# Performance work log

Measured on AMD Instinct MI355X. Metric: run time of the kernel, lower is better.

## Reference

```python
import jax, jax.numpy as jnp
import numpy as np

DIM = 1024
N = 65536

def _l2norm(x):
    # F.normalize: x / max(||x||_2, eps) along last dim, eps=1e-12
    n = jnp.linalg.norm(x, axis=-1, keepdims=True)
    return x / jnp.maximum(n, 1e-12)

def setup_inputs() -> dict:
    key = jax.random.key(0)
    ks = jax.random.split(key, 10)
    s = 0.02
    return {
        "q_init": jax.random.normal(ks[0], (1, DIM), jnp.float32),
        "k_init": jax.random.normal(ks[1], (N, DIM), jnp.float32),
        "Wq": jax.random.normal(ks[2], (DIM, DIM // 2), jnp.float32) * s,
        "bq": jnp.zeros((DIM // 2,), jnp.float32),
        "Wk": jax.random.normal(ks[3], (DIM, DIM // 2), jnp.float32) * s,
        "bk": jnp.zeros((DIM // 2,), jnp.float32),
        "Wv": jax.random.normal(ks[4], (DIM, DIM), jnp.float32) * s,
        "bv": jnp.zeros((DIM,), jnp.float32),
        "Wm": jax.random.normal(ks[5], (DIM, DIM), jnp.float32) * s,
        "bm": jnp.zeros((DIM,), jnp.float32),
        "gamma": jnp.ones((1,), jnp.float32),
    }

def reference(q_init, k_init, Wq, bq, Wk, bk, Wv, bv, Wm, bm, gamma):
    q = _l2norm(q_init) @ Wq + bq              # [1, dim/2]
    kn = _l2norm(k_init)                        # [N, dim]
    k = kn @ Wk + bk                            # [N, dim/2]
    v = kn @ Wv + bv                            # [N, dim]
    scores = q @ k.T                            # [1, N]
    # global mean/std rescale (torch.std is unbiased, ddof=1)
    scores = (scores - scores.mean()) / (jnp.std(scores, ddof=1) + 1e-8)
    attn = jax.nn.softmax(jnp.clip(scores, -10.0, 10.0), axis=-1)
    # dropout is identity in eval mode
    out = (attn @ v) @ Wm + bm                  # [1, dim]
    g = jax.nn.sigmoid(gamma)                   # [1]
    return g * q_init + (1.0 - g) * out
```

## Files before the change

kernel.cpp:

```cpp
#include <hip/hip_runtime.h>
#include <math.h>

#define DIM   1024
#define HALF  512
#define NROWS 65536
#define SBLK  4096
#define WBLK  2048
#define WF1   64

#define OFF_SCAL   0
#define OFF_QACC   (OFF_SCAL + 8)
#define OFF_PVEC   (OFF_QACC + HALF)
#define OFF_PSTAT  (OFF_PVEC + DIM)
#define OFF_S      (OFF_PSTAT + 2*SBLK)
#define OFF_INVN   (OFF_S + NROWS)
#define OFF_PESUM  (OFF_INVN + NROWS)
#define OFF_PW     (OFF_PESUM + WBLK)
#define OFF_P2     (OFF_PW + WBLK*DIM)
#define OFF_WACC   (OFF_P2 + WF1*DIM)
#define OFF_OVACC  (OFF_WACC + DIM)
#define OFF_END    (OFF_OVACC + DIM)

__global__ void k_prep(const float* __restrict__ q_init,
                       const float* __restrict__ Wq,
                       float* __restrict__ qacc) {
    __shared__ float qs[DIM];
    __shared__ float4 red4[256];
    __shared__ float red[256];
    int t = threadIdx.x, c4 = blockIdx.x;
    float sq = 0.f;
    #pragma unroll
    for (int i = 0; i < 4; ++i) {
        float v = q_init[t + i * 256];
        qs[t + i * 256] = v;
        sq += v * v;
    }
    red[t] = sq;
    __syncthreads();
    for (int s = 128; s > 0; s >>= 1) {
        if (t < s) red[t] += red[t + s];
        __syncthreads();
    }
    float inv = 1.0f / fmaxf(sqrtf(red[0]), 1e-12f);
    const float4* W4 = (const float4*)Wq;
    float4 acc = make_float4(0.f, 0.f, 0.f, 0.f);
    for (int r = t; r < DIM; r += 256) {
        float c = qs[r] * inv;
        float4 m = W4[(size_t)r * (HALF / 4) + c4];
        acc.x += c * m.x; acc.y += c * m.y; acc.z += c * m.z; acc.w += c * m.w;
    }
    red4[t] = acc;
    __syncthreads();
    for (int s = 128; s > 0; s >>= 1) {
        if (t < s) {
            red4[t].x += red4[t + s].x; red4[t].y += red4[t + s].y;
            red4[t].z += red4[t + s].z; red4[t].w += red4[t + s].w;
        }
        __syncthreads();
    }
    if (t == 0) ((float4*)qacc)[c4] = red4[0];
}

__global__ void k_pvec(const float* __restrict__ Wk,
                       const float* __restrict__ qacc,
                       const float* __restrict__ bq,
                       float* __restrict__ pvec) {
    __shared__ float q[HALF];
    int t = threadIdx.x;
    for (int j = t; j < HALF; j += 256) q[j] = qacc[j] + bq[j];
    __syncthreads();
    int wave = t >> 6, lane = t & 63;
    int d = blockIdx.x * 4 + wave;
    const float* row = Wk + (size_t)d * HALF;
    float acc = 0.f;
    #pragma unroll
    for (int j0 = 0; j0 < HALF; j0 += 64) acc += row[j0 + lane] * q[j0 + lane];
    #pragma unroll
    for (int o = 32; o > 0; o >>= 1) acc += __shfl_down(acc, o);
    if (lane == 0) pvec[d] = acc;
}

__global__ void k_scores(const float* __restrict__ K,
                         const float* __restrict__ pvec,
                         float* __restrict__ svals,
                         float* __restrict__ invn,
                         float2* __restrict__ pstat) {
    __shared__ float4 p4s[256];
    __shared__ float wsum[4], wssq[4];
    int t = threadIdx.x;
    p4s[t] = ((const float4*)pvec)[t];
    __syncthreads();
    int wave = t >> 6, lane = t & 63;
    int row0 = blockIdx.x * 16 + wave * 4;
    const float4* k4 = (const float4*)K + (size_t)row0 * 256 + lane;
    float4 v[16];
    #pragma unroll
    for (int r = 0; r < 4; ++r)
        #pragma unroll
        for (int i = 0; i < 4; ++i)
            v[r * 4 + i] = k4[r * 256 + i * 64];
    float d[4] = {0, 0, 0, 0}, q[4] = {0, 0, 0, 0};
    #pragma unroll
    for (int r = 0; r < 4; ++r) {
        #pragma unroll
        for (int i = 0; i < 4; ++i) {
            float4 a = v[r * 4 + i];
            float4 p = p4s[lane + i * 64];
            d[r] += a.x * p.x + a.y * p.y + a.z * p.z + a.w * p.w;
            q[r] += a.x * a.x + a.y * a.y + a.z * a.z + a.w * a.w;
        }
    }
    #pragma unroll
    for (int o = 32; o > 0; o >>= 1) {
        #pragma unroll
        for (int r = 0; r < 4; ++r) {
            d[r] += __shfl_down(d[r], o);
            q[r] += __shfl_down(q[r], o);
        }
    }
    if (lane == 0) {
        float i0 = 1.0f / fmaxf(sqrtf(q[0]), 1e-12f);
        float i1 = 1.0f / fmaxf(sqrtf(q[1]), 1e-12f);
        float i2 = 1.0f / fmaxf(sqrtf(q[2]), 1e-12f);
        float i3 = 1.0f / fmaxf(sqrtf(q[3]), 1e-12f);
        float s0 = d[0] * i0, s1 = d[1] * i1, s2 = d[2] * i2, s3 = d[3] * i3;
        *(float4*)(svals + row0) = make_float4(s0, s1, s2, s3);
        *(float4*)(invn + row0) = make_float4(i0, i1, i2, i3);
        wsum[wave] = s0 + s1 + s2 + s3;
        wssq[wave] = s0 * s0 + s1 * s1 + s2 * s2 + s3 * s3;
    }
    __syncthreads();
    if (t == 0)
        pstat[blockIdx.x] = make_float2(wsum[0] + wsum[1] + wsum[2] + wsum[3],
                                        wssq[0] + wssq[1] + wssq[2] + wssq[3]);
}

__global__ void k_redstats(const float2* __restrict__ pstat, float* __restrict__ scal) {
    __shared__ float rs[1024], rq[1024];
    int t = threadIdx.x;
    float s = 0.f, q = 0.f;
    for (int i = t; i < SBLK; i += 1024) {
        float2 p = pstat[i];
        s += p.x; q += p.y;
    }
    rs[t] = s; rq[t] = q;
    __syncthreads();
    for (int k = 512; k > 0; k >>= 1) {
        if (t < k) { rs[t] += rs[t + k]; rq[t] += rq[t + k]; }
        __syncthreads();
    }
    if (t == 0) {
        float mean = rs[0] / (float)NROWS;
        float var  = (rq[0] - (float)NROWS * mean * mean) / (float)(NROWS - 1);
        scal[0] = mean;
        scal[1] = 1.0f / (sqrtf(fmaxf(var, 0.0f)) + 1e-8f);
    }
}

__global__ void k_wsum(const float* __restrict__ K,
                       const float* __restrict__ svals,
                       const float* __restrict__ invn,
                       const float* __restrict__ scal,
                       float* __restrict__ pw,
                       float* __restrict__ pesum) {
    int t = threadIdx.x;
    int b = (int)gridDim.x - 1 - (int)blockIdx.x;
    int r0 = b * 32;
    float mean = scal[0], rstd = scal[1];
    const float4* M4 = (const float4*)K + (size_t)r0 * 256 + t;
    float4 acc = make_float4(0.f, 0.f, 0.f, 0.f);
    float esum = 0.f;
    #pragma unroll
    for (int rb = 0; rb < 32; rb += 8) {
        float4 m[8];
        #pragma unroll
        for (int r = 0; r < 8; ++r) m[r] = M4[(size_t)(rb + r) * 256];
        #pragma unroll
        for (int r = 0; r < 8; ++r) {
            int ri = r0 + rb + r;
            float z = (svals[ri] - mean) * rstd;
            z = fminf(fmaxf(z, -10.0f), 10.0f);
            float e = expf(z);
            esum += e;
            float c = e * invn[ri];
            acc.x += c * m[r].x; acc.y += c * m[r].y;
            acc.z += c * m[r].z; acc.w += c * m[r].w;
        }
    }
    ((float4*)pw)[(size_t)b * 256 + t] = acc;
    if (t == 0) pesum[b] = esum;
}

__global__ void k_wfold(const float* __restrict__ pw, float* __restrict__ p2) {
    int t = threadIdx.x, b = blockIdx.x;
    const float4* pw4 = (const float4*)pw;
    float4 acc = make_float4(0.f, 0.f, 0.f, 0.f);
    #pragma unroll
    for (int p = 0; p < WBLK / WF1; ++p) {
        float4 m = pw4[(size_t)(b * (WBLK / WF1) + p) * 256 + t];
        acc.x += m.x; acc.y += m.y; acc.z += m.z; acc.w += m.w;
    }
    ((float4*)p2)[b * 256 + t] = acc;
}

__global__ void k_wreduce(const float* __restrict__ p2,
                          const float* __restrict__ pesum,
                          float* __restrict__ wacc) {
    __shared__ float red[1024];
    int t = threadIdx.x;
    float es = 0.f;
    for (int i = t; i < WBLK; i += 1024) es += pesum[i];
    red[t] = es;
    __syncthreads();
    for (int s = 512; s > 0; s >>= 1) {
        if (t < s) red[t] += red[t + s];
        __syncthreads();
    }
    float inv = 1.0f / red[0];
    float acc = 0.f;
    #pragma unroll
    for (int b = 0; b < WF1; ++b) acc += p2[b * DIM + t];
    wacc[t] = acc * inv;
}

__global__ void k_mv(const float* __restrict__ M,
                     const float* __restrict__ coeff,
                     const float* __restrict__ cbias,
                     float* __restrict__ out) {
    __shared__ float4 red[256];
    int t = threadIdx.x, c4 = blockIdx.x;
    const float4* M4 = (const float4*)M;
    float4 acc = make_float4(0.f, 0.f, 0.f, 0.f);
    for (int r = t; r < DIM; r += 256) {
        float c = coeff[r];
        if (cbias) c += cbias[r];
        float4 m = M4[(size_t)r * (DIM / 4) + c4];
        acc.x += c * m.x; acc.y += c * m.y; acc.z += c * m.z; acc.w += c * m.w;
    }
    red[t] = acc;
    __syncthreads();
    for (int s = 128; s > 0; s >>= 1) {
        if (t < s) {
            red[t].x += red[t + s].x; red[t].y += red[t + s].y;
            red[t].z += red[t + s].z; red[t].w += red[t + s].w;
        }
        __syncthreads();
    }
    if (t == 0) ((float4*)out)[c4] = red[0];
}

__global__ void k_mv_final(const float* __restrict__ M,
                           const float* __restrict__ coeff,
                           const float* __restrict__ cbias,
                           const float* __restrict__ q_init,
                           const float* __restrict__ bm,
                           const float* __restrict__ gamma,
                           float* __restrict__ out) {
    __shared__ float4 red[256];
    int t = threadIdx.x, c4 = blockIdx.x;
    const float4* M4 = (const float4*)M;
    float4 acc = make_float4(0.f, 0.f, 0.f, 0.f);
    for (int r = t; r < DIM; r += 256) {
        float c = coeff[r] + cbias[r];
        float4 m = M4[(size_t)r * (DIM / 4) + c4];
        acc.x += c * m.x; acc.y += c * m.y; acc.z += c * m.z; acc.w += c * m.w;
    }
    red[t] = acc;
    __syncthreads();
    for (int s = 128; s > 0; s >>= 1) {
        if (t < s) {
            red[t].x += red[t + s].x; red[t].y += red[t + s].y;
            red[t].z += red[t + s].z; red[t].w += red[t + s].w;
        }
        __syncthreads();
    }
    if (t == 0) {
        float g = 1.0f / (1.0f + expf(-gamma[0]));
        float4 qv = ((const float4*)q_init)[c4];
        float4 bmv = ((const float4*)bm)[c4];
        float4 o;
        o.x = g * qv.x + (1.0f - g) * (red[0].x + bmv.x);
        o.y = g * qv.y + (1.0f - g) * (red[0].y + bmv.y);
        o.z = g * qv.z + (1.0f - g) * (red[0].z + bmv.z);
        o.w = g * qv.w + (1.0f - g) * (red[0].w + bmv.w);
        ((float4*)out)[c4] = o;
    }
}

extern "C" void kernel_launch(void* const* d_in, const int* in_sizes, int n_in,
                              void* d_out, int out_size, void* d_ws, size_t ws_size,
                              hipStream_t stream) {
    const float* q_init = (const float*)d_in[0];
    const float* k_init = (const float*)d_in[1];
    const float* Wq     = (const float*)d_in[2];
    const float* bq     = (const float*)d_in[3];
    const float* Wk     = (const float*)d_in[4];
    const float* Wv     = (const float*)d_in[6];
    const float* bv     = (const float*)d_in[7];
    const float* Wm     = (const float*)d_in[8];
    const float* bm     = (const float*)d_in[9];
    const float* gamma  = (const float*)d_in[10];
    float* out = (float*)d_out;
    float* ws  = (float*)d_ws;

    float*  scal   = ws + OFF_SCAL;
    float*  qacc   = ws + OFF_QACC;
    float*  pvec   = ws + OFF_PVEC;
    float2* pstat  = (float2*)(ws + OFF_PSTAT);
    float*  svals  = ws + OFF_S;
    float*  invn   = ws + OFF_INVN;
    float*  pesum  = ws + OFF_PESUM;
    float*  pw     = ws + OFF_PW;
    float*  p2     = ws + OFF_P2;
    float*  wacc   = ws + OFF_WACC;
    float*  ovacc  = ws + OFF_OVACC;

    k_prep<<<HALF / 4, 256, 0, stream>>>(q_init, Wq, qacc);
    k_pvec<<<DIM / 4, 256, 0, stream>>>(Wk, qacc, bq, pvec);
    k_scores<<<SBLK, 256, 0, stream>>>(k_init, pvec, svals, invn, pstat);
    k_redstats<<<1, 1024, 0, stream>>>(pstat, scal);
    k_wsum<<<WBLK, 256, 0, stream>>>(k_init, svals, invn, scal, pw, pesum);
    k_wfold<<<WF1, 256, 0, stream>>>(pw, p2);
    k_wreduce<<<1, 1024, 0, stream>>>(p2, pesum, wacc);
    k_mv<<<DIM / 4, 256, 0, stream>>>(Wv, wacc, nullptr, ovacc);
    k_mv_final<<<DIM / 4, 256, 0, stream>>>(Wm, ovacc, bv, q_init, bm, gamma, out);
}
```

Measured before the change: 472.5 us.

## Fuse all stages into one cooperative persistent kernel with grid syncs

Replaces the nine-kernel pipeline with a single cooperative kernel of 512 blocks that separates the stages with grid.sync(). The scores and weighted-sum stages each process 128 rows per block, and the multi-level partial-sum folds collapse into one cross-block reduction. The aim is to remove launch overhead and intermediate round trips, and to keep the 256MB K matrix partly resident in cache between the two passes because each block rereads its own rows. In exchange it adds six grid-wide barriers and leaves fewer blocks in flight for hiding memory latency during the streaming passes.

```diff
diff --git a/kernel.cpp b/kernel.cpp
--- a/kernel.cpp
+++ b/kernel.cpp
@@ -1,289 +1,279 @@
 #include <hip/hip_runtime.h>
+#include <hip/hip_cooperative_groups.h>
 #include <math.h>
+
+namespace cg = cooperative_groups;
 
 #define DIM   1024
 #define HALF  512
 #define NROWS 65536
-#define SBLK  4096
-#define WBLK  2048
-#define WF1   64
-
-#define OFF_SCAL   0
-#define OFF_QACC   (OFF_SCAL + 8)
-#define OFF_PVEC   (OFF_QACC + HALF)
-#define OFF_PSTAT  (OFF_PVEC + DIM)
-#define OFF_S      (OFF_PSTAT + 2*SBLK)
-#define OFF_INVN   (OFF_S + NROWS)
-#define OFF_PESUM  (OFF_INVN + NROWS)
-#define OFF_PW     (OFF_PESUM + WBLK)
-#define OFF_P2     (OFF_PW + WBLK*DIM)
-#define OFF_WACC   (OFF_P2 + WF1*DIM)
-#define OFF_OVACC  (OFF_WACC + DIM)
-#define OFF_END    (OFF_OVACC + DIM)
-
-__global__ void k_prep(const float* __restrict__ q_init,
-                       const float* __restrict__ Wq,
-                       float* __restrict__ qacc) {
-    __shared__ float qs[DIM];
-    __shared__ float4 red4[256];
-    __shared__ float red[256];
-    int t = threadIdx.x, c4 = blockIdx.x;
-    float sq = 0.f;
-    #pragma unroll
-    for (int i = 0; i < 4; ++i) {
-        float v = q_init[t + i * 256];
-        qs[t + i * 256] = v;
-        sq += v * v;
-    }
-    red[t] = sq;
+#define NB    512
+#define RPB   128
+
+#define OFF_QACC  0
+#define OFF_PVEC  512
+#define OFF_PSTAT 1536
+#define OFF_SV    2560
+#define OFF_INVN  (OFF_SV + NROWS)
+#define OFF_PESUM (OFF_INVN + NROWS)
+#define OFF_PW    (OFF_PESUM + NB)
+#define OFF_WACC  (OFF_PW + NB * DIM)
+#define OFF_OV    (OFF_WACC + DIM)
+
+__device__ __forceinline__ void f4acc(float4& a, float c, const float4& m) {
+    a.x += c * m.x; a.y += c * m.y; a.z += c * m.z; a.w += c * m.w;
+}
+
+__global__ __launch_bounds__(256, 2)
+void k_fused(const float* __restrict__ q_init, const float* __restrict__ k_init,
+             const float* __restrict__ Wq, const float* __restrict__ bq,
+             const float* __restrict__ Wk, const float* __restrict__ Wv,
+             const float* __restrict__ bv, const float* __restrict__ Wm,
+             const float* __restrict__ bm, const float* __restrict__ gamma,
+             float* __restrict__ ws, float* __restrict__ out)
+{
+    cg::grid_group grid = cg::this_grid();
+    __shared__ float  s_f[1280];
+    __shared__ float4 s_v4[256];
+    const int t = threadIdx.x;
+    const int b = blockIdx.x;
+    const int wave = t >> 6, lane = t & 63;
+
+    float*  qacc  = ws + OFF_QACC;
+    float*  pvec  = ws + OFF_PVEC;
+    float2* pstat = (float2*)(ws + OFF_PSTAT);
+    float*  svals = ws + OFF_SV;
+    float*  invn  = ws + OFF_INVN;
+    float*  pesum = ws + OFF_PESUM;
+    float*  pw    = ws + OFF_PW;
+    float*  wacc  = ws + OFF_WACC;
+    float*  ovacc = ws + OFF_OV;
+
+    if (b < HALF / 4) {
+        float sq = 0.f;
+        #pragma unroll
+        for (int i = 0; i < 4; ++i) {
+            float v = q_init[t + i * 256];
+            s_f[t + i * 256] = v;
+            sq += v * v;
+        }
+        s_f[1024 + t] = sq;
+        __syncthreads();
+        for (int s = 128; s > 0; s >>= 1) {
+            if (t < s) s_f[1024 + t] += s_f[1024 + t + s];
+            __syncthreads();
+        }
+        float inv = 1.0f / fmaxf(sqrtf(s_f[1024]), 1e-12f);
+        const float4* W4 = (const float4*)Wq;
+        float4 acc = make_float4(0.f, 0.f, 0.f, 0.f);
+        #pragma unroll
+        for (int i = 0; i < 4; ++i) {
+            int r = t + i * 256;
+            f4acc(acc, s_f[r] * inv, W4[(size_t)r * (HALF / 4) + b]);
+        }
+        s_v4[t] = acc;
+        __syncthreads();
+        for (int s = 128; s > 0; s >>= 1) {
+            if (t < s) {
+                s_v4[t].x += s_v4[t + s].x; s_v4[t].y += s_v4[t + s].y;
+                s_v4[t].z += s_v4[t + s].z; s_v4[t].w += s_v4[t + s].w;
+            }
+            __syncthreads();
+        }
+        if (t == 0) ((float4*)qacc)[b] = s_v4[0];
+    }
+    grid.sync();
+
+    if (b < 256) {
+        if (t < 128) {
+            float4 qa = ((const float4*)qacc)[t];
+            float4 bb = ((const float4*)bq)[t];
+            s_v4[t] = make_float4(qa.x + bb.x, qa.y + bb.y, qa.z + bb.z, qa.w + bb.w);
+        }
+        __syncthreads();
+        int d = b * 4 + wave;
+        const float4* row4 = (const float4*)(Wk + (size_t)d * HALF);
+        float acc = 0.f;
+        #pragma unroll
+        for (int i = 0; i < 2; ++i) {
+            float4 a = row4[lane + 64 * i];
+            float4 p = s_v4[lane + 64 * i];
+            acc += a.x * p.x + a.y * p.y + a.z * p.z + a.w * p.w;
+        }
+        #pragma unroll
+        for (int o = 32; o > 0; o >>= 1) acc += __shfl_down(acc, o);
+        if (lane == 0) pvec[d] = acc;
+    }
+    grid.sync();
+
+    s_v4[t] = ((const float4*)pvec)[t];
     __syncthreads();
-    for (int s = 128; s > 0; s >>= 1) {
-        if (t < s) red[t] += red[t + s];
-        __syncthreads();
-    }
-    float inv = 1.0f / fmaxf(sqrtf(red[0]), 1e-12f);
-    const float4* W4 = (const float4*)Wq;
-    float4 acc = make_float4(0.f, 0.f, 0.f, 0.f);
-    for (int r = t; r < DIM; r += 256) {
-        float c = qs[r] * inv;
-        float4 m = W4[(size_t)r * (HALF / 4) + c4];
-        acc.x += c * m.x; acc.y += c * m.y; acc.z += c * m.z; acc.w += c * m.w;
-    }
-    red4[t] = acc;
-    __syncthreads();
-    for (int s = 128; s > 0; s >>= 1) {
-        if (t < s) {
-            red4[t].x += red4[t + s].x; red4[t].y += red4[t + s].y;
-            red4[t].z += red4[t + s].z; red4[t].w += red4[t + s].w;
-        }
-        __syncthreads();
-    }
-    if (t == 0) ((float4*)qacc)[c4] = red4[0];
-}
-
-__global__ void k_pvec(const float* __restrict__ Wk,
-                       const float* __restrict__ qacc,
-                       const float* __restrict__ bq,
-                       float* __restrict__ pvec) {
-    __shared__ float q[HALF];
-    int t = threadIdx.x;
-    for (int j = t; j < HALF; j += 256) q[j] = qacc[j] + bq[j];
-    __syncthreads();
-    int wave = t >> 6, lane = t & 63;
-    int d = blockIdx.x * 4 + wave;
-    const float* row = Wk + (size_t)d * HALF;
-    float acc = 0.f;
-    #pragma unroll
-    for (int j0 = 0; j0 < HALF; j0 += 64) acc += row[j0 + lane] * q[j0 + lane];
-    #pragma unroll
-    for (int o = 32; o > 0; o >>= 1) acc += __shfl_down(acc, o);
-    if (lane == 0) pvec[d] = acc;
-}
-
-__global__ void k_scores(const float* __restrict__ K,
-                         const float* __restrict__ pvec,
-                         float* __restrict__ svals,
-                         float* __restrict__ invn,
-                         float2* __restrict__ pstat) {
-    __shared__ float4 p4s[256];
-    __shared__ float wsum[4], wssq[4];
-    int t = threadIdx.x;
-    p4s[t] = ((const float4*)pvec)[t];
-    __syncthreads();
-    int wave = t >> 6, lane = t & 63;
-    int row0 = blockIdx.x * 16 + wave * 4;
-    const float4* k4 = (const float4*)K + (size_t)row0 * 256 + lane;
-    float4 v[16];
-    #pragma unroll
-    for (int r = 0; r < 4; ++r)
-        #pragma unroll
-        for (int i = 0; i < 4; ++i)
-            v[r * 4 + i] = k4[r * 256 + i * 64];
-    float d[4] = {0, 0, 0, 0}, q[4] = {0, 0, 0, 0};
-    #pragma unroll
-    for (int r = 0; r < 4; ++r) {
-        #pragma unroll
-        for (int i = 0; i < 4; ++i) {
-            float4 a = v[r * 4 + i];
-            float4 p = p4s[lane + i * 64];
-            d[r] += a.x * p.x + a.y * p.y + a.z * p.z + a.w * p.w;
-            q[r] += a.x * a.x + a.y * a.y + a.z * a.z + a.w * a.w;
-        }
-    }
-    #pragma unroll
-    for (int o = 32; o > 0; o >>= 1) {
-        #pragma unroll
-        for (int r = 0; r < 4; ++r) {
-            d[r] += __shfl_down(d[r], o);
-            q[r] += __shfl_down(q[r], o);
-        }
-    }
-    if (lane == 0) {
-        float i0 = 1.0f / fmaxf(sqrtf(q[0]), 1e-12f);
-        float i1 = 1.0f / fmaxf(sqrtf(q[1]), 1e-12f);
-        float i2 = 1.0f / fmaxf(sqrtf(q[2]), 1e-12f);
-        float i3 = 1.0f / fmaxf(sqrtf(q[3]), 1e-12f);
-        float s0 = d[0] * i0, s1 = d[1] * i1, s2 = d[2] * i2, s3 = d[3] * i3;
-        *(float4*)(svals + row0) = make_float4(s0, s1, s2, s3);
-        *(float4*)(invn + row0) = make_float4(i0, i1, i2, i3);
-        wsum[wave] = s0 + s1 + s2 + s3;
-        wssq[wave] = s0 * s0 + s1 * s1 + s2 * s2 + s3 * s3;
-    }
-    __syncthreads();
-    if (t == 0)
-        pstat[blockIdx.x] = make_float2(wsum[0] + wsum[1] + wsum[2] + wsum[3],
-                                        wssq[0] + wssq[1] + wssq[2] + wssq[3]);
-}
-
-__global__ void k_redstats(const float2* __restrict__ pstat, float* __restrict__ scal) {
-    __shared__ float rs[1024], rq[1024];
-    int t = threadIdx.x;
-    float s = 0.f, q = 0.f;
-    for (int i = t; i < SBLK; i += 1024) {
-        float2 p = pstat[i];
-        s += p.x; q += p.y;
-    }
-    rs[t] = s; rq[t] = q;
-    __syncthreads();
-    for (int k = 512; k > 0; k >>= 1) {
-        if (t < k) { rs[t] += rs[t + k]; rq[t] += rq[t + k]; }
-        __syncthreads();
-    }
-    if (t == 0) {
-        float mean = rs[0] / (float)NROWS;
-        float var  = (rq[0] - (float)NROWS * mean * mean) / (float)(NROWS - 1);
-        scal[0] = mean;
-        scal[1] = 1.0f / (sqrtf(fmaxf(var, 0.0f)) + 1e-8f);
-    }
-}
-
-__global__ void k_wsum(const float* __restrict__ K,
-                       const float* __restrict__ svals,
-                       const float* __restrict__ invn,
-                       const float* __restrict__ scal,
-                       float* __restrict__ pw,
-                       float* __restrict__ pesum) {
-    int t = threadIdx.x;
-    int b = (int)gridDim.x - 1 - (int)blockIdx.x;
-    int r0 = b * 32;
-    float mean = scal[0], rstd = scal[1];
-    const float4* M4 = (const float4*)K + (size_t)r0 * 256 + t;
-    float4 acc = make_float4(0.f, 0.f, 0.f, 0.f);
-    float esum = 0.f;
-    #pragma unroll
-    for (int rb = 0; rb < 32; rb += 8) {
-        float4 m[8];
-        #pragma unroll
-        for (int r = 0; r < 8; ++r) m[r] = M4[(size_t)(rb + r) * 256];
-        #pragma unroll
-        for (int r = 0; r < 8; ++r) {
-            int ri = r0 + rb + r;
-            float z = (svals[ri] - mean) * rstd;
-            z = fminf(fmaxf(z, -10.0f), 10.0f);
-            float e = expf(z);
-            esum += e;
-            float c = e * invn[ri];
-            acc.x += c * m[r].x; acc.y += c * m[r].y;
-            acc.z += c * m[r].z; acc.w += c * m[r].w;
-        }
-    }
-    ((float4*)pw)[(size_t)b * 256 + t] = acc;
-    if (t == 0) pesum[b] = esum;
-}
-
-__global__ void k_wfold(const float* __restrict__ pw, float* __restrict__ p2) {
-    int t = threadIdx.x, b = blockIdx.x;
-    const float4* pw4 = (const float4*)pw;
-    float4 acc = make_float4(0.f, 0.f, 0.f, 0.f);
-    #pragma unroll
-    for (int p = 0; p < WBLK / WF1; ++p) {
-        float4 m = pw4[(size_t)(b * (WBLK / WF1) + p) * 256 + t];
-        acc.x += m.x; acc.y += m.y; acc.z += m.z; acc.w += m.w;
-    }
-    ((float4*)p2)[b * 256 + t] = acc;
-}
-
-__global__ void k_wreduce(const float* __restrict__ p2,
-                          const float* __restrict__ pesum,
-                          float* __restrict__ wacc) {
-    __shared__ float red[1024];
-    int t = threadIdx.x;
-    float es = 0.f;
-    for (int i = t; i < WBLK; i += 1024) es += pesum[i];
-    red[t] = es;
-    __syncthreads();
-    for (int s = 512; s > 0; s >>= 1) {
-        if (t < s) red[t] += red[t + s];
-        __syncthreads();
-    }
-    float inv = 1.0f / red[0];
-    float acc = 0.f;
-    #pragma unroll
-    for (int b = 0; b < WF1; ++b) acc += p2[b * DIM + t];
-    wacc[t] = acc * inv;
-}
-
-__global__ void k_mv(const float* __restrict__ M,
-                     const float* __restrict__ coeff,
-                     const float* __restrict__ cbias,
-                     float* __restrict__ out) {
-    __shared__ float4 red[256];
-    int t = threadIdx.x, c4 = blockIdx.x;
-    const float4* M4 = (const float4*)M;
-    float4 acc = make_float4(0.f, 0.f, 0.f, 0.f);
-    for (int r = t; r < DIM; r += 256) {
-        float c = coeff[r];
-        if (cbias) c += cbias[r];
-        float4 m = M4[(size_t)r * (DIM / 4) + c4];
-        acc.x += c * m.x; acc.y += c * m.y; acc.z += c * m.z; acc.w += c * m.w;
-    }
-    red[t] = acc;
-    __syncthreads();
-    for (int s = 128; s > 0; s >>= 1) {
-        if (t < s) {
-            red[t].x += red[t + s].x; red[t].y += red[t + s].y;
-            red[t].z += red[t + s].z; red[t].w += red[t + s].w;
-        }
-        __syncthreads();
-    }
-    if (t == 0) ((float4*)out)[c4] = red[0];
-}
-
-__global__ void k_mv_final(const float* __restrict__ M,
-                           const float* __restrict__ coeff,
-                           const float* __restrict__ cbias,
-                           const float* __restrict__ q_init,
-                           const float* __restrict__ bm,
-                           const float* __restrict__ gamma,
-                           float* __restrict__ out) {
-    __shared__ float4 red[256];
-    int t = threadIdx.x, c4 = blockIdx.x;
-    const float4* M4 = (const float4*)M;
-    float4 acc = make_float4(0.f, 0.f, 0.f, 0.f);
-    for (int r = t; r < DIM; r += 256) {
-        float c = coeff[r] + cbias[r];
-        float4 m = M4[(size_t)r * (DIM / 4) + c4];
-        acc.x += c * m.x; acc.y += c * m.y; acc.z += c * m.z; acc.w += c * m.w;
-    }
-    red[t] = acc;
-    __syncthreads();
-    for (int s = 128; s > 0; s >>= 1) {
-        if (t < s) {
-            red[t].x += red[t + s].x; red[t].y += red[t + s].y;
-            red[t].z += red[t + s].z; red[t].w += red[t + s].w;
-        }
-        __syncthreads();
-    }
-    if (t == 0) {
-        float g = 1.0f / (1.0f + expf(-gamma[0]));
-        float4 qv = ((const float4*)q_init)[c4];
-        float4 bmv = ((const float4*)bm)[c4];
-        float4 o;
-        o.x = g * qv.x + (1.0f - g) * (red[0].x + bmv.x);
-        o.y = g * qv.y + (1.0f - g) * (red[0].y + bmv.y);
-        o.z = g * qv.z + (1.0f - g) * (red[0].z + bmv.z);
-        o.w = g * qv.w + (1.0f - g) * (red[0].w + bmv.w);
-        ((float4*)out)[c4] = o;
+    {
+        int base = b * RPB + wave * 32;
+        float wsum = 0.f, wssq = 0.f;
+        for (int g2 = 0; g2 < 8; ++g2) {
+            int row0 = base + g2 * 4;
+            const float4* k4 = (const float4*)k_init + (size_t)row0 * 256 + lane;
+            float4 v[16];
+            #pragma unroll
+            for (int r = 0; r < 4; ++r)
+                #pragma unroll
+                for (int i = 0; i < 4; ++i)
+                    v[r * 4 + i] = k4[r * 256 + i * 64];
+            float d4[4] = {0, 0, 0, 0}, q4[4] = {0, 0, 0, 0};
+            #pragma unroll
+            for (int r = 0; r < 4; ++r) {
+                #pragma unroll
+                for (int i = 0; i < 4; ++i) {
+                    float4 a = v[r * 4 + i];
+                    float4 p = s_v4[lane + i * 64];
+                    d4[r] += a.x * p.x + a.y * p.y + a.z * p.z + a.w * p.w;
+                    q4[r] += a.x * a.x + a.y * a.y + a.z * a.z + a.w * a.w;
+                }
+            }
+            #pragma unroll
+            for (int o = 32; o > 0; o >>= 1) {
+                #pragma unroll
+                for (int r = 0; r < 4; ++r) {
+                    d4[r] += __shfl_down(d4[r], o);
+                    q4[r] += __shfl_down(q4[r], o);
+                }
+            }
+            if (lane == 0) {
+                float i0 = 1.0f / fmaxf(sqrtf(q4[0]), 1e-12f);
+                float i1 = 1.0f / fmaxf(sqrtf(q4[1]), 1e-12f);
+                float i2 = 1.0f / fmaxf(sqrtf(q4[2]), 1e-12f);
+                float i3 = 1.0f / fmaxf(sqrtf(q4[3]), 1e-12f);
+                float s0 = d4[0] * i0, s1 = d4[1] * i1, s2 = d4[2] * i2, s3 = d4[3] * i3;
+                *(float4*)(svals + row0) = make_float4(s0, s1, s2, s3);
+                *(float4*)(invn + row0)  = make_float4(i0, i1, i2, i3);
+                wsum += s0 + s1 + s2 + s3;
+                wssq += s0 * s0 + s1 * s1 + s2 * s2 + s3 * s3;
+            }
+        }
+        if (lane == 0) { s_f[wave] = wsum; s_f[4 + wave] = wssq; }
+        __syncthreads();
+        if (t == 0)
+            pstat[b] = make_float2(s_f[0] + s_f[1] + s_f[2] + s_f[3],
+                                   s_f[4] + s_f[5] + s_f[6] + s_f[7]);
+    }
+    grid.sync();
+
+    {
+        float2 pa = pstat[t], pb = pstat[t + 256];
+        s_f[t] = pa.x + pb.x;
+        s_f[256 + t] = pa.y + pb.y;
+        __syncthreads();
+        for (int s = 128; s > 0; s >>= 1) {
+            if (t < s) { s_f[t] += s_f[t + s]; s_f[256 + t] += s_f[256 + t + s]; }
+            __syncthreads();
+        }
+        if (t == 0) {
+            float mean = s_f[0] / (float)NROWS;
+            float var  = (s_f[256] - (float)NROWS * mean * mean) / (float)(NROWS - 1);
+            s_f[512] = mean;
+            s_f[513] = 1.0f / (sqrtf(fmaxf(var, 0.0f)) + 1e-8f);
+        }
+        __syncthreads();
+    }
+    float mean = s_f[512], rstd = s_f[513];
+
+    {
+        int r0 = b * RPB;
+        const float4* K4 = (const float4*)k_init + (size_t)r0 * 256 + t;
+        float4 acc = make_float4(0.f, 0.f, 0.f, 0.f);
+        float esum = 0.f;
+        for (int gb = 15; gb >= 0; --gb) {
+            float4 m[8];
+            #pragma unroll
+            for (int r = 0; r < 8; ++r) m[r] = K4[(size_t)(gb * 8 + r) * 256];
+            #pragma unroll
+            for (int r = 0; r < 8; ++r) {
+                int ri = r0 + gb * 8 + r;
+                float z = (svals[ri] - mean) * rstd;
+                z = fminf(fmaxf(z, -10.0f), 10.0f);
+                float e = expf(z);
+                esum += e;
+                f4acc(acc, e * invn[ri], m[r]);
+            }
+        }
+        ((float4*)pw)[(size_t)b * 256 + t] = acc;
+        if (t == 0) pesum[b] = esum;
+    }
+    grid.sync();
+
+    if (b < 256) {
+        const float4* pw4 = (const float4*)pw;
+        float4 a0 = pw4[(size_t)t * 256 + b];
+        float4 a1 = pw4[(size_t)(t + 256) * 256 + b];
+        s_v4[t] = make_float4(a0.x + a1.x, a0.y + a1.y, a0.z + a1.z, a0.w + a1.w);
+        s_f[t] = pesum[t] + pesum[t + 256];
+        __syncthreads();
+        for (int s = 128; s > 0; s >>= 1) {
+            if (t < s) {
+                s_v4[t].x += s_v4[t + s].x; s_v4[t].y += s_v4[t + s].y;
+                s_v4[t].z += s_v4[t + s].z; s_v4[t].w += s_v4[t + s].w;
+                s_f[t] += s_f[t + s];
+            }
+            __syncthreads();
+        }
+        if (t == 0) {
+            float inv = 1.0f / s_f[0];
+            float4 w = s_v4[0];
+            ((float4*)wacc)[b] = make_float4(w.x * inv, w.y * inv, w.z * inv, w.w * inv);
+        }
+    }
+    grid.sync();
+
+    if (b < 256) {
+        const float4* W4 = (const float4*)Wv;
+        float4 acc = make_float4(0.f, 0.f, 0.f, 0.f);
+        #pragma unroll
+        for (int i = 0; i < 4; ++i) {
+            int r = t + i * 256;
+            f4acc(acc, wacc[r], W4[(size_t)r * 256 + b]);
+        }
+        s_v4[t] = acc;
+        __syncthreads();
+        for (int s = 128; s > 0; s >>= 1) {
+            if (t < s) {
+                s_v4[t].x += s_v4[t + s].x; s_v4[t].y += s_v4[t + s].y;
+                s_v4[t].z += s_v4[t + s].z; s_v4[t].w += s_v4[t + s].w;
+            }
+            __syncthreads();
+        }
+        if (t == 0) ((float4*)ovacc)[b] = s_v4[0];
+    }
+    grid.sync();
+
+    if (b < 256) {
+        const float4* W4 = (const float4*)Wm;
+        float4 acc = make_float4(0.f, 0.f, 0.f, 0.f);
+        #pragma unroll
+        for (int i = 0; i < 4; ++i) {
+            int r = t + i * 256;
+            f4acc(acc, ovacc[r] + bv[r], W4[(size_t)r * 256 + b]);
+        }
+        s_v4[t] = acc;
+        __syncthreads();
+        for (int s = 128; s > 0; s >>= 1) {
+            if (t < s) {
+                s_v4[t].x += s_v4[t + s].x; s_v4[t].y += s_v4[t + s].y;
+                s_v4[t].z += s_v4[t + s].z; s_v4[t].w += s_v4[t + s].w;
+            }
+            __syncthreads();
+        }
+        if (t == 0) {
+            float gv = 1.0f / (1.0f + expf(-gamma[0]));
+            float4 qv  = ((const float4*)q_init)[b];
+            float4 bmv = ((const float4*)bm)[b];
+            float4 red = s_v4[0];
+            ((float4*)out)[b] = make_float4(
+                gv * qv.x + (1.0f - gv) * (red.x + bmv.x),
+                gv * qv.y + (1.0f - gv) * (red.y + bmv.y),
+                gv * qv.z + (1.0f - gv) * (red.z + bmv.z),
+                gv * qv.w + (1.0f - gv) * (red.w + bmv.w));
+        }
     }
 }
 
@@ -303,25 +293,7 @@
     float* out = (float*)d_out;
     float* ws  = (float*)d_ws;
 
-    float*  scal   = ws + OFF_SCAL;
-    float*  qacc   = ws + OFF_QACC;
-    float*  pvec   = ws + OFF_PVEC;
-    float2* pstat  = (float2*)(ws + OFF_PSTAT);
-    float*  svals  = ws + OFF_S;
-    float*  invn   = ws + OFF_INVN;
-    float*  pesum  = ws + OFF_PESUM;
-    float*  pw     = ws + OFF_PW;
-    float*  p2     = ws + OFF_P2;
-    float*  wacc   = ws + OFF_WACC;
-    float*  ovacc  = ws + OFF_OVACC;
-
-    k_prep<<<HALF / 4, 256, 0, stream>>>(q_init, Wq, qacc);
-    k_pvec<<<DIM / 4, 256, 0, stream>>>(Wk, qacc, bq, pvec);
-    k_scores<<<SBLK, 256, 0, stream>>>(k_init, pvec, svals, invn, pstat);
-    k_redstats<<<1, 1024, 0, stream>>>(pstat, scal);
-    k_wsum<<<WBLK, 256, 0, stream>>>(k_init, svals, invn, scal, pw, pesum);
-    k_wfold<<<WF1, 256, 0, stream>>>(pw, p2);
-    k_wreduce<<<1, 1024, 0, stream>>>(p2, pesum, wacc);
-    k_mv<<<DIM / 4, 256, 0, stream>>>(Wv, wacc, nullptr, ovacc);
-    k_mv_final<<<DIM / 4, 256, 0, stream>>>(Wm, ovacc, bv, q_init, bm, gamma, out);
+    void* args[] = { &q_init, &k_init, &Wq, &bq, &Wk, &Wv, &bv, &Wm, &bm,
+                     &gamma, &ws, &out };
+    hipLaunchCooperativeKernel((void*)k_fused, dim3(NB), dim3(256), args, 0, stream);
 }
```

Result: slower. 819.3 us (+73.4%).
